# Kernel optimization log

Hardware: AMD Instinct MI355X
Metric: run time of the kernel (lower is better)

Reference implementation:

```python
import jax, jax.numpy as jnp
import numpy as np

NUM_EXPERTS = 8
TOP_K = 2
RMS_EPS = 1e-6
SCALING = NUM_EXPERTS / TOP_K


def setup_inputs() -> dict:
    key = jax.random.key(0)
    ks = jax.random.split(key, 6)
    B, S, H, I, E = 4, 2048, 2048, 1024, NUM_EXPERTS
    return {
        "hidden_states": jax.random.normal(ks[0], (B, S, H), dtype=jnp.float32),
        "norm_w": jnp.ones((H,), dtype=jnp.float32),
        "router_w": jax.random.normal(ks[1], (E, H), dtype=jnp.float32) * 0.02,
        "gate_w": jax.random.normal(ks[2], (E, I, H), dtype=jnp.float32) * 0.02,
        "up_w": jax.random.normal(ks[3], (E, I, H), dtype=jnp.float32) * 0.02,
        "down_w": jax.random.normal(ks[4], (E, H, I), dtype=jnp.float32) * 0.02,
    }


def reference(hidden_states, norm_w, router_w, gate_w, up_w, down_w):
    B, S, H = hidden_states.shape
    T = B * S
    flat = hidden_states.reshape(T, H)

    # RMSNorm on router input (fp32 math, as in torch module)
    x32 = flat.astype(jnp.float32)
    var = jnp.mean(x32 * x32, axis=-1, keepdims=True)
    router_input = norm_w * (x32 * jax.lax.rsqrt(var + RMS_EPS))

    # Router: softmax -> top-k -> renormalize
    logits = router_input @ router_w.T                     # [T, E]
    probs = jax.nn.softmax(logits, axis=-1)
    topw, topi = jax.lax.top_k(probs, TOP_K)               # [T, K]
    topw = topw / jnp.sum(topw, axis=-1, keepdims=True)

    # Expert combine: per-token weight for expert e (0 if not selected).
    # Running every token through every expert with weight-0 masking is
    # mathematically identical to the gather/scatter dispatch.
    out = jnp.zeros_like(flat)
    for e in range(NUM_EXPERTS):
        w_e = jnp.sum(jnp.where(topi == e, topw, 0.0), axis=-1)   # [T]
        g = flat @ gate_w[e].T                                    # [T, I]
        u = flat @ up_w[e].T                                      # [T, I]
        o = (jax.nn.silu(g) * u) @ down_w[e].T                    # [T, H]
        out = out + o * w_e[:, None]

    student_output = out.reshape(B, S, H) * SCALING

    # Aux load-balancing loss (training path)
    importance = jnp.sum(probs, axis=0) / T                       # [E]
    load = jnp.sum(topi[..., None] == jnp.arange(NUM_EXPERTS), axis=(0, 1)) / (T * TOP_K)
    aux_loss = jnp.sum(importance * load.astype(jnp.float32)) * NUM_EXPERTS

    return student_output, aux_loss
```

## Files before the change

### kernel.cpp

```cpp
#include <hip/hip_runtime.h>
#include <hip/hip_bf16.h>
#include <cstdint>

#define T_TOKENS 8192
#define H_DIM 2048
#define I_DIM 1024
#define N_EXPERTS 8
#define PAIRS (T_TOKENS * 2)
#define TOT_TILES 144
#define TOT_ROWS (TOT_TILES * 128)

using f32x4 = __attribute__((ext_vector_type(4))) float;
using bfv   = __attribute__((ext_vector_type(8))) short;
using u16x8 = __attribute__((ext_vector_type(8))) unsigned short;

typedef __attribute__((address_space(3))) unsigned int lds_u32;
typedef __attribute__((address_space(1))) unsigned int glb_u32;

__device__ __forceinline__ void gll16(const void* g, void* l) {
  __builtin_amdgcn_global_load_lds((const glb_u32*)g, (lds_u32*)l, 16, 0, 0);
}
#define SB0() __builtin_amdgcn_sched_barrier(0)
#define BAR() __builtin_amdgcn_s_barrier()

__device__ inline unsigned short f2bf(float f) {
  unsigned int u = __float_as_uint(f);
  u += 0x7FFFu + ((u >> 16) & 1u);
  return (unsigned short)(u >> 16);
}
__device__ inline float bf2f(unsigned short u) {
  return __uint_as_float((unsigned int)u << 16);
}

__global__ __launch_bounds__(256) void moe_convert_kernel(
    const float* __restrict__ src, unsigned short* __restrict__ dst, int n8) {
  int i = blockIdx.x * 256 + threadIdx.x;
  if (i >= n8) return;
  size_t o = (size_t)i * 8;
  f32x4 a = *reinterpret_cast<const f32x4*>(src + o);
  f32x4 b = *reinterpret_cast<const f32x4*>(src + o + 4);
  u16x8 r = {f2bf(a[0]), f2bf(a[1]), f2bf(a[2]), f2bf(a[3]),
             f2bf(b[0]), f2bf(b[1]), f2bf(b[2]), f2bf(b[3])};
  *reinterpret_cast<u16x8*>(dst + o) = r;
}

__global__ __launch_bounds__(256) void moe_router_kernel(
    const float* __restrict__ X, const float* __restrict__ norm_w,
    const float* __restrict__ rw, float* __restrict__ probs,
    float* __restrict__ topw, int* __restrict__ topi,
    unsigned int* __restrict__ counts, unsigned short* __restrict__ Xb,
    const float* __restrict__ gate_w, const float* __restrict__ up_w,
    const float* __restrict__ down_w,
    unsigned short* __restrict__ W1, unsigned short* __restrict__ W2,
    unsigned short* __restrict__ W3) {
  int t = blockIdx.x;
  int tid = threadIdx.x;
  {
    size_t co = (size_t)t * 2048 + tid * 8;
    f32x4 a = *reinterpret_cast<const f32x4*>(gate_w + co);
    f32x4 b = *reinterpret_cast<const f32x4*>(gate_w + co + 4);
    u16x8 r = {f2bf(a[0]), f2bf(a[1]), f2bf(a[2]), f2bf(a[3]),
               f2bf(b[0]), f2bf(b[1]), f2bf(b[2]), f2bf(b[3])};
    *reinterpret_cast<u16x8*>(W1 + co) = r;
    a = *reinterpret_cast<const f32x4*>(up_w + co);
    b = *reinterpret_cast<const f32x4*>(up_w + co + 4);
    u16x8 r2 = {f2bf(a[0]), f2bf(a[1]), f2bf(a[2]), f2bf(a[3]),
                f2bf(b[0]), f2bf(b[1]), f2bf(b[2]), f2bf(b[3])};
    *reinterpret_cast<u16x8*>(W2 + co) = r2;
    if (W3) {
      a = *reinterpret_cast<const f32x4*>(down_w + co);
      b = *reinterpret_cast<const f32x4*>(down_w + co + 4);
      u16x8 r3 = {f2bf(a[0]), f2bf(a[1]), f2bf(a[2]), f2bf(a[3]),
                  f2bf(b[0]), f2bf(b[1]), f2bf(b[2]), f2bf(b[3])};
      *reinterpret_cast<u16x8*>(W3 + co) = r3;
    }
  }
  const float* x = X + (size_t)t * H_DIM;
  int base = tid * 8;
  f32x4 v0 = *reinterpret_cast<const f32x4*>(x + base);
  f32x4 v1 = *reinterpret_cast<const f32x4*>(x + base + 4);
  u16x8 bx = {f2bf(v0[0]), f2bf(v0[1]), f2bf(v0[2]), f2bf(v0[3]),
              f2bf(v1[0]), f2bf(v1[1]), f2bf(v1[2]), f2bf(v1[3])};
  *reinterpret_cast<u16x8*>(Xb + (size_t)t * H_DIM + base) = bx;
  f32x4 nw0 = *reinterpret_cast<const f32x4*>(norm_w + base);
  f32x4 nw1 = *reinterpret_cast<const f32x4*>(norm_w + base + 4);
  float vals[9];
  vals[0] = v0[0]*v0[0] + v0[1]*v0[1] + v0[2]*v0[2] + v0[3]*v0[3]
          + v1[0]*v1[0] + v1[1]*v1[1] + v1[2]*v1[2] + v1[3]*v1[3];
  f32x4 a0 = v0 * nw0, a1 = v1 * nw1;
#pragma unroll
  for (int e = 0; e < 8; ++e) {
    const float* r = rw + e * H_DIM + base;
    f32x4 r0 = *reinterpret_cast<const f32x4*>(r);
    f32x4 r1 = *reinterpret_cast<const f32x4*>(r + 4);
    f32x4 d = a0 * r0 + a1 * r1;
    vals[e + 1] = d[0] + d[1] + d[2] + d[3];
  }
#pragma unroll
  for (int v = 0; v < 9; ++v) {
    float s = vals[v];
#pragma unroll
    for (int off = 32; off > 0; off >>= 1) s += __shfl_xor(s, off);
    vals[v] = s;
  }
  __shared__ float red[4][9];
  int lane = tid & 63, w = tid >> 6;
  if (lane == 0) {
#pragma unroll
    for (int v = 0; v < 9; ++v) red[w][v] = vals[v];
  }
  __syncthreads();
  if (tid == 0) {
    float tot[9];
#pragma unroll
    for (int v = 0; v < 9; ++v) tot[v] = red[0][v] + red[1][v] + red[2][v] + red[3][v];
    float rs = rsqrtf(tot[0] / (float)H_DIM + 1e-6f);
    float lg[8], mx = -1e30f;
#pragma unroll
    for (int e = 0; e < 8; ++e) { lg[e] = tot[e + 1] * rs; mx = fmaxf(mx, lg[e]); }
    float pe[8], sum = 0.f;
#pragma unroll
    for (int e = 0; e < 8; ++e) { pe[e] = expf(lg[e] - mx); sum += pe[e]; }
    float inv = 1.f / sum;
#pragma unroll
    for (int e = 0; e < 8; ++e) { pe[e] *= inv; probs[t * 8 + e] = pe[e]; }
    int b1 = 0; float p1 = pe[0];
#pragma unroll
    for (int e = 1; e < 8; ++e) if (pe[e] > p1) { p1 = pe[e]; b1 = e; }
    int b2 = -1; float p2 = -1.f;
#pragma unroll
    for (int e = 0; e < 8; ++e) if (e != b1 && pe[e] > p2) { p2 = pe[e]; b2 = e; }
    float wsum = p1 + p2;
    topw[t * 2] = p1 / wsum;
    topw[t * 2 + 1] = p2 / wsum;
    topi[t * 2] = b1;
    topi[t * 2 + 1] = b2;
    atomicAdd(&counts[b1], 1u);
    atomicAdd(&counts[8 + b2], 1u);
  }
}

__global__ __launch_bounds__(256) void moe_importance_kernel(
    const float* __restrict__ probs, float* __restrict__ impSum) {
  int e = blockIdx.x, tid = threadIdx.x;
  float s = 0.f;
  for (int t = tid; t < T_TOKENS; t += 256) s += probs[t * 8 + e];
  __shared__ float red[256];
  red[tid] = s;
  __syncthreads();
  for (int st = 128; st > 0; st >>= 1) {
    if (tid < st) red[tid] += red[tid + st];
    __syncthreads();
  }
  if (tid == 0) impSum[e] = red[0];
}

__global__ void moe_offsets_aux_kernel(const unsigned int* __restrict__ counts,
                                       const float* __restrict__ impSum,
                                       int* __restrict__ tileOff,
                                       float* __restrict__ out_aux) {
  if (threadIdx.x == 0 && blockIdx.x == 0) {
    int acc = 0;
    for (int b = 0; b < 16; ++b) {
      tileOff[b] = acc;
      acc += (int)((counts[b] + 127u) >> 7);
    }
    tileOff[16] = acc;
    float a = 0.f;
    for (int e = 0; e < 8; ++e) {
      float load = (float)(counts[e] + counts[8 + e]) / (float)PAIRS;
      a += (impSum[e] / (float)T_TOKENS) * load;
    }
    out_aux[0] = a * (float)N_EXPERTS;
  }
}

__global__ __launch_bounds__(256) void moe_assign_kernel(
    const int* __restrict__ topi, const int* __restrict__ tileOff,
    unsigned int* __restrict__ cursors, int* __restrict__ row2pair) {
  int p = blockIdx.x * 256 + threadIdx.x;
  if (p >= PAIRS) return;
  int b = topi[p] + 8 * (p & 1);
  unsigned int pos = atomicAdd(&cursors[b], 1u);
  row2pair[tileOff[b] * 128 + (int)pos] = p;
}


__global__ __launch_bounds__(256, 2) void moe_stage_a(
    const unsigned short* __restrict__ Xb,
    const unsigned short* __restrict__ Wg, const unsigned short* __restrict__ Wu,
    const int* __restrict__ row2pair, const int* __restrict__ tileOff,
    unsigned int* __restrict__ workCtr, unsigned short* __restrict__ P) {
  __shared__ __align__(16) unsigned short sAB[2][16384];
  __shared__ int sTok[128];
  __shared__ int sWork;
  const int tid = threadIdx.x;
  const int lane = tid & 63, w = tid >> 6;
  const int wm = w >> 1, wn = w & 1;
  const int lrow = lane & 15, grp = lane >> 4;
  const int sub = lane >> 3;
  const int kcs = ((lane & 7) ^ sub) << 3;
  const int cx = (lane & 7) << 3;
  const int nTiles = tileOff[16];
  const int nWork = nTiles * 16;

  for (;;) {
    if (tid == 0) sWork = (int)atomicAdd(workCtr, 1u);
    __syncthreads();
    const int item = sWork;
    if (item >= nWork) break;
    const int mt = item % nTiles;
    const int nt = item / nTiles;
    int b = 0;
#pragma unroll
    for (int k = 1; k < 16; ++k) if (tileOff[k] <= mt) b = k;
    const int e = b & 7;
    const int row0 = mt * 128;
    if (tid < 128) {
      int pr = row2pair[row0 + tid];
      sTok[tid] = (pr >= 0) ? (pr >> 1) : 0;
    }
    __syncthreads();

    const size_t wbase = (size_t)e * ((size_t)I_DIM * H_DIM);
    const unsigned short* src[8];
#pragma unroll
    for (int i = 0; i < 4; ++i) {
      int row = i * 32 + 8 * w + sub;
      src[i] = Xb + (size_t)sTok[row] * H_DIM + kcs;
    }
#pragma unroll
    for (int i = 4; i < 8; ++i) {
      int brow = (i - 4) * 32 + 8 * w + sub;
      int wq = brow >> 6, r6 = brow & 63;
      int ic = nt * 64 + wq * 32 + (r6 & 31);
      const unsigned short* bp = (r6 & 32) ? Wu : Wg;
      src[i] = bp + wbase + (size_t)ic * H_DIM + kcs;
    }

    f32x4 acc[4][4] = {};

#pragma unroll
    for (int i = 0; i < 8; ++i)
      gll16(src[i], (void*)&sAB[0][(i * 256 + tid) * 8]);

    int cur = 0;
#pragma unroll 1
    for (int kk = 0; kk < 32; ++kk) {
      if (kk < 31) {
#pragma unroll
        for (int i = 0; i < 8; ++i)
          gll16(src[i] + ((kk + 1) << 6), (void*)&sAB[cur ^ 1][(i * 256 + tid) * 8]);
        SB0();
        asm volatile("s_waitcnt vmcnt(8)" ::: "memory");
      } else {
        asm volatile("s_waitcnt vmcnt(0)" ::: "memory");
      }
      SB0();
      BAR();
      SB0();
#pragma unroll
      for (int ks = 0; ks < 2; ++ks) {
        const int co = ((ks * 4 + grp) << 3) ^ cx;
        bfv af[4], bf[4];
#pragma unroll
        for (int m = 0; m < 4; ++m)
          af[m] = *reinterpret_cast<const bfv*>(
              &sAB[cur][(wm * 64 + m * 16 + lrow) * 64 + co]);
#pragma unroll
        for (int n = 0; n < 4; ++n)
          bf[n] = *reinterpret_cast<const bfv*>(
              &sAB[cur][8192 + (wn * 64 + n * 16 + lrow) * 64 + co]);
        __builtin_amdgcn_s_setprio(1);
#pragma unroll
        for (int m = 0; m < 4; ++m)
#pragma unroll
          for (int n = 0; n < 4; ++n)
            acc[m][n] = __builtin_amdgcn_mfma_f32_16x16x32_bf16(af[m], bf[n], acc[m][n], 0, 0, 0);
        __builtin_amdgcn_s_setprio(0);
      }
      SB0();
      BAR();
      cur ^= 1;
    }

#pragma unroll
    for (int m = 0; m < 4; ++m) {
#pragma unroll
      for (int n = 0; n < 2; ++n) {
#pragma unroll
        for (int j = 0; j < 4; ++j) {
          float g = acc[m][n][j];
          float uu = acc[m][n + 2][j];
          float pv = (g / (1.f + expf(-g))) * uu;
          int row = row0 + wm * 64 + m * 16 + grp * 4 + j;
          int col = nt * 64 + wn * 32 + n * 16 + lrow;
          P[(size_t)row * I_DIM + col] = f2bf(pv);
        }
      }
    }
  }
}

__global__ __launch_bounds__(256, 2) void moe_stage_b(
    const unsigned short* __restrict__ Pb, const unsigned short* __restrict__ Wd,
    const int* __restrict__ row2pair, const int* __restrict__ tileOff,
    unsigned int* __restrict__ workCtr, unsigned short* __restrict__ Opairs) {
  __shared__ __align__(16) unsigned short sAB[2][16384];
  __shared__ int sPair[128];
  __shared__ int sWork;
  const int tid = threadIdx.x;
  const int lane = tid & 63, w = tid >> 6;
  const int wm = w >> 1, wn = w & 1;
  const int lrow = lane & 15, grp = lane >> 4;
  const int sub = lane >> 3;
  const int kcs = ((lane & 7) ^ sub) << 3;
  const int cx = (lane & 7) << 3;
  const int nTiles = tileOff[16];
  const int nWork = nTiles * 16;

  for (;;) {
    if (tid == 0) sWork = (int)atomicAdd(workCtr, 1u);
    __syncthreads();
    const int item = sWork;
    if (item >= nWork) break;
    const int mt = item % nTiles;
    const int nt = item / nTiles;
    int b = 0;
#pragma unroll
    for (int k = 1; k < 16; ++k) if (tileOff[k] <= mt) b = k;
    const int e = b & 7;
    const int row0 = mt * 128, h0 = nt * 128;
    if (tid < 128) sPair[tid] = row2pair[row0 + tid];
    __syncthreads();

    const unsigned short* src[8];
#pragma unroll
    for (int i = 0; i < 4; ++i) {
      int row = i * 32 + 8 * w + sub;
      src[i] = Pb + (size_t)(row0 + row) * I_DIM + kcs;
    }
#pragma unroll
    for (int i = 4; i < 8; ++i) {
      int brow = (i - 4) * 32 + 8 * w + sub;
      src[i] = Wd + (size_t)e * ((size_t)H_DIM * I_DIM) + (size_t)(h0 + brow) * I_DIM + kcs;
    }

    f32x4 acc[4][4] = {};

#pragma unroll
    for (int i = 0; i < 8; ++i)
      gll16(src[i], (void*)&sAB[0][(i * 256 + tid) * 8]);

    int cur = 0;
#pragma unroll 1
    for (int kk = 0; kk < 16; ++kk) {
      if (kk < 15) {
#pragma unroll
        for (int i = 0; i < 8; ++i)
          gll16(src[i] + ((kk + 1) << 6), (void*)&sAB[cur ^ 1][(i * 256 + tid) * 8]);
        SB0();
        asm volatile("s_waitcnt vmcnt(8)" ::: "memory");
      } else {
        asm volatile("s_waitcnt vmcnt(0)" ::: "memory");
      }
      SB0();
      BAR();
      SB0();
#pragma unroll
      for (int ks = 0; ks < 2; ++ks) {
        const int co = ((ks * 4 + grp) << 3) ^ cx;
        bfv af[4], bf[4];
#pragma unroll
        for (int m = 0; m < 4; ++m)
          af[m] = *reinterpret_cast<const bfv*>(
              &sAB[cur][(wm * 64 + m * 16 + lrow) * 64 + co]);
#pragma unroll
        for (int n = 0; n < 4; ++n)
          bf[n] = *reinterpret_cast<const bfv*>(
              &sAB[cur][8192 + (wn * 64 + n * 16 + lrow) * 64 + co]);
        __builtin_amdgcn_s_setprio(1);
#pragma unroll
        for (int m = 0; m < 4; ++m)
#pragma unroll
          for (int n = 0; n < 4; ++n)
            acc[m][n] = __builtin_amdgcn_mfma_f32_16x16x32_bf16(af[m], bf[n], acc[m][n], 0, 0, 0);
        __builtin_amdgcn_s_setprio(0);
      }
      SB0();
      BAR();
      cur ^= 1;
    }

#pragma unroll
    for (int m = 0; m < 4; ++m) {
#pragma unroll
      for (int j = 0; j < 4; ++j) {
        int rl = wm * 64 + m * 16 + grp * 4 + j;
        int pr = sPair[rl];
        if (pr < 0) continue;
        unsigned short* orow = Opairs + (size_t)pr * H_DIM + h0 + wn * 64 + lrow;
#pragma unroll
        for (int n = 0; n < 4; ++n) orow[n * 16] = f2bf(acc[m][n][j]);
      }
    }
  }
}

__global__ __launch_bounds__(256) void moe_combine_kernel(
    const unsigned short* __restrict__ Opairs, const float* __restrict__ topw,
    float* __restrict__ out) {
  size_t g = (size_t)blockIdx.x * 256 + threadIdx.x;
  size_t base = g * 8;
  int t = (int)(base >> 11);
  int h = (int)(base & 2047);
  float w0 = topw[t * 2] * 4.f;
  float w1 = topw[t * 2 + 1] * 4.f;
  u16x8 o0 = *reinterpret_cast<const u16x8*>(Opairs + (size_t)(t * 2) * H_DIM + h);
  u16x8 o1 = *reinterpret_cast<const u16x8*>(Opairs + (size_t)(t * 2 + 1) * H_DIM + h);
  f32x4 r0, r1;
#pragma unroll
  for (int j = 0; j < 4; ++j) r0[j] = w0 * bf2f(o0[j]) + w1 * bf2f(o1[j]);
#pragma unroll
  for (int j = 0; j < 4; ++j) r1[j] = w0 * bf2f(o0[4 + j]) + w1 * bf2f(o1[4 + j]);
  *reinterpret_cast<f32x4*>(out + base) = r0;
  *reinterpret_cast<f32x4*>(out + base + 4) = r1;
}

extern "C" void kernel_launch(void* const* d_in, const int* in_sizes, int n_in,
                              void* d_out, int out_size, void* d_ws, size_t ws_size,
                              hipStream_t stream) {
  const float* X = (const float*)d_in[0];
  const float* norm_w = (const float*)d_in[1];
  const float* router_w = (const float*)d_in[2];
  const float* gate_w = (const float*)d_in[3];
  const float* up_w = (const float*)d_in[4];
  const float* down_w = (const float*)d_in[5];
  float* out = (float*)d_out;

  char* ws = (char*)d_ws;
  unsigned short* P = (unsigned short*)(ws);
  float* probs = (float*)(ws + 37748736);
  float* topw = (float*)(ws + 38010880);
  int* topi = (int*)(ws + 38076416);
  int* row2pair = (int*)(ws + 38141952);
  char* ctrl = ws + 38215680;
  unsigned int* counts = (unsigned int*)(ctrl);
  unsigned int* cursors = (unsigned int*)(ctrl + 64);
  float* impSum = (float*)(ctrl + 128);
  int* tileOff = (int*)(ctrl + 192);
  unsigned int* wcA = (unsigned int*)(ctrl + 384);
  unsigned int* wcB = (unsigned int*)(ctrl + 388);
  unsigned short* W1 = (unsigned short*)(ws + 38216192);
  unsigned short* W2 = (unsigned short*)(ws + 71770624);
  unsigned short* Xb = (unsigned short*)(ws + 105325056);
  unsigned short* Opairs = (unsigned short*)(ws + 71770624);
  unsigned short* W3 = (unsigned short*)(ws + 138879488);
  const bool w3ok = ws_size >= 172433920ull;

  hipMemsetAsync(ctrl, 0, 512, stream);
  hipMemsetAsync(row2pair, 0xFF, (size_t)TOT_ROWS * 4, stream);

  moe_router_kernel<<<T_TOKENS, 256, 0, stream>>>(
      X, norm_w, router_w, probs, topw, topi, counts, Xb,
      gate_w, up_w, down_w, W1, W2, w3ok ? W3 : nullptr);
  moe_importance_kernel<<<N_EXPERTS, 256, 0, stream>>>(probs, impSum);
  moe_offsets_aux_kernel<<<1, 64, 0, stream>>>(counts, impSum, tileOff, out + 16777216);
  moe_assign_kernel<<<PAIRS / 256, 256, 0, stream>>>(topi, tileOff, cursors, row2pair);

  moe_stage_a<<<512, 256, 0, stream>>>(Xb, W1, W2, row2pair, tileOff, wcA, P);

  const unsigned short* DW = W3;
  if (!w3ok) {
    const int N8 = (N_EXPERTS * I_DIM * H_DIM) / 8;
    moe_convert_kernel<<<N8 / 256, 256, 0, stream>>>(down_w, W1, N8);
    DW = W1;
  }
  moe_stage_b<<<512, 256, 0, stream>>>(P, DW, row2pair, tileOff, wcB, Opairs);
  moe_combine_kernel<<<T_TOKENS, 256, 0, stream>>>(Opairs, topw, out);
}
```

Measured before the change: 626.4 us.

## Drop LDS double buffering to run four blocks per CU in expert GEMMs

Both expert GEMM stages switch from a double-buffered LDS pipeline to a single 32KB buffer with a synchronous load-then-compute loop. Launch bounds and grid size double so four blocks can share a CU and hide latency through occupancy rather than software prefetch. Work items are also reordered so consecutive items walk the N tiles of one M tile, which improves reuse of the activation rows. The cost is that each block now stalls on its own loads every K step, and register pressure under the tighter launch bound may cause spills.

```diff
diff --git a/kernel.cpp b/kernel.cpp
--- a/kernel.cpp
+++ b/kernel.cpp
@@ -186,12 +186,12 @@
 }
 
 
-__global__ __launch_bounds__(256, 2) void moe_stage_a(
+__global__ __launch_bounds__(256, 4) void moe_stage_a(
     const unsigned short* __restrict__ Xb,
     const unsigned short* __restrict__ Wg, const unsigned short* __restrict__ Wu,
     const int* __restrict__ row2pair, const int* __restrict__ tileOff,
     unsigned int* __restrict__ workCtr, unsigned short* __restrict__ P) {
-  __shared__ __align__(16) unsigned short sAB[2][16384];
+  __shared__ __align__(16) unsigned short sAB[16384];
   __shared__ int sTok[128];
   __shared__ int sWork;
   const int tid = threadIdx.x;
@@ -209,8 +209,8 @@
     __syncthreads();
     const int item = sWork;
     if (item >= nWork) break;
-    const int mt = item % nTiles;
-    const int nt = item / nTiles;
+    const int mt = item >> 4;
+    const int nt = item & 15;
     int b = 0;
 #pragma unroll
     for (int k = 1; k < 16; ++k) if (tileOff[k] <= mt) b = k;
@@ -240,22 +240,13 @@
 
     f32x4 acc[4][4] = {};
 
-#pragma unroll
-    for (int i = 0; i < 8; ++i)
-      gll16(src[i], (void*)&sAB[0][(i * 256 + tid) * 8]);
-
-    int cur = 0;
 #pragma unroll 1
     for (int kk = 0; kk < 32; ++kk) {
-      if (kk < 31) {
-#pragma unroll
-        for (int i = 0; i < 8; ++i)
-          gll16(src[i] + ((kk + 1) << 6), (void*)&sAB[cur ^ 1][(i * 256 + tid) * 8]);
-        SB0();
-        asm volatile("s_waitcnt vmcnt(8)" ::: "memory");
-      } else {
-        asm volatile("s_waitcnt vmcnt(0)" ::: "memory");
-      }
+#pragma unroll
+      for (int i = 0; i < 8; ++i)
+        gll16(src[i] + (kk << 6), (void*)&sAB[(i * 256 + tid) * 8]);
+      SB0();
+      asm volatile("s_waitcnt vmcnt(0)" ::: "memory");
       SB0();
       BAR();
       SB0();
@@ -266,11 +257,11 @@
 #pragma unroll
         for (int m = 0; m < 4; ++m)
           af[m] = *reinterpret_cast<const bfv*>(
-              &sAB[cur][(wm * 64 + m * 16 + lrow) * 64 + co]);
+              &sAB[(wm * 64 + m * 16 + lrow) * 64 + co]);
 #pragma unroll
         for (int n = 0; n < 4; ++n)
           bf[n] = *reinterpret_cast<const bfv*>(
-              &sAB[cur][8192 + (wn * 64 + n * 16 + lrow) * 64 + co]);
+              &sAB[8192 + (wn * 64 + n * 16 + lrow) * 64 + co]);
         __builtin_amdgcn_s_setprio(1);
 #pragma unroll
         for (int m = 0; m < 4; ++m)
@@ -281,7 +272,6 @@
       }
       SB0();
       BAR();
-      cur ^= 1;
     }
 
 #pragma unroll
@@ -302,11 +292,11 @@
   }
 }
 
-__global__ __launch_bounds__(256, 2) void moe_stage_b(
+__global__ __launch_bounds__(256, 4) void moe_stage_b(
     const unsigned short* __restrict__ Pb, const unsigned short* __restrict__ Wd,
     const int* __restrict__ row2pair, const int* __restrict__ tileOff,
     unsigned int* __restrict__ workCtr, unsigned short* __restrict__ Opairs) {
-  __shared__ __align__(16) unsigned short sAB[2][16384];
+  __shared__ __align__(16) unsigned short sAB[16384];
   __shared__ int sPair[128];
   __shared__ int sWork;
   const int tid = threadIdx.x;
@@ -324,8 +314,8 @@
     __syncthreads();
     const int item = sWork;
     if (item >= nWork) break;
-    const int mt = item % nTiles;
-    const int nt = item / nTiles;
+    const int mt = item >> 4;
+    const int nt = item & 15;
     int b = 0;
 #pragma unroll
     for (int k = 1; k < 16; ++k) if (tileOff[k] <= mt) b = k;
@@ -348,22 +338,13 @@
 
     f32x4 acc[4][4] = {};
 
-#pragma unroll
-    for (int i = 0; i < 8; ++i)
-      gll16(src[i], (void*)&sAB[0][(i * 256 + tid) * 8]);
-
-    int cur = 0;
 #pragma unroll 1
     for (int kk = 0; kk < 16; ++kk) {
-      if (kk < 15) {
-#pragma unroll
-        for (int i = 0; i < 8; ++i)
-          gll16(src[i] + ((kk + 1) << 6), (void*)&sAB[cur ^ 1][(i * 256 + tid) * 8]);
-        SB0();
-        asm volatile("s_waitcnt vmcnt(8)" ::: "memory");
-      } else {
-        asm volatile("s_waitcnt vmcnt(0)" ::: "memory");
-      }
+#pragma unroll
+      for (int i = 0; i < 8; ++i)
+        gll16(src[i] + (kk << 6), (void*)&sAB[(i * 256 + tid) * 8]);
+      SB0();
+      asm volatile("s_waitcnt vmcnt(0)" ::: "memory");
       SB0();
       BAR();
       SB0();
@@ -374,11 +355,11 @@
 #pragma unroll
         for (int m = 0; m < 4; ++m)
           af[m] = *reinterpret_cast<const bfv*>(
-              &sAB[cur][(wm * 64 + m * 16 + lrow) * 64 + co]);
+              &sAB[(wm * 64 + m * 16 + lrow) * 64 + co]);
 #pragma unroll
         for (int n = 0; n < 4; ++n)
           bf[n] = *reinterpret_cast<const bfv*>(
-              &sAB[cur][8192 + (wn * 64 + n * 16 + lrow) * 64 + co]);
+              &sAB[8192 + (wn * 64 + n * 16 + lrow) * 64 + co]);
         __builtin_amdgcn_s_setprio(1);
 #pragma unroll
         for (int m = 0; m < 4; ++m)
@@ -389,7 +370,6 @@
       }
       SB0();
       BAR();
-      cur ^= 1;
     }
 
 #pragma unroll
@@ -468,7 +448,7 @@
   moe_offsets_aux_kernel<<<1, 64, 0, stream>>>(counts, impSum, tileOff, out + 16777216);
   moe_assign_kernel<<<PAIRS / 256, 256, 0, stream>>>(topi, tileOff, cursors, row2pair);
 
-  moe_stage_a<<<512, 256, 0, stream>>>(Xb, W1, W2, row2pair, tileOff, wcA, P);
+  moe_stage_a<<<1024, 256, 0, stream>>>(Xb, W1, W2, row2pair, tileOff, wcA, P);
 
   const unsigned short* DW = W3;
   if (!w3ok) {
@@ -476,6 +456,6 @@
     moe_convert_kernel<<<N8 / 256, 256, 0, stream>>>(down_w, W1, N8);
     DW = W1;
   }
-  moe_stage_b<<<512, 256, 0, stream>>>(P, DW, row2pair, tileOff, wcB, Opairs);
+  moe_stage_b<<<1024, 256, 0, stream>>>(P, DW, row2pair, tileOff, wcB, Opairs);
   moe_combine_kernel<<<T_TOKENS, 256, 0, stream>>>(Opairs, topw, out);
 }
```

Result: no change. 623.2 us (-0.5%).
